# Kernel tuning notes

Hardware: AMD Instinct MI355X
Metric: run time of the kernel (lower is better)

The kernel has to match this reference:

```python
import jax, jax.numpy as jnp
import numpy as np

V, B, NT, EN, EMB, ODIM = 5000, 512, 50, 200, 200, 40
PERP = 30.0
BETA_TEMP = 0.2
SINKHORN_ALPHA = 20.0
WEIGHT_ECR = 250.0
ECR_ITERS = 100
SNE_ITERS = 20
EPS_DIV = 1e-16


def _pairwise_sq(x, y):
    # ||x_i||^2 + ||y_j||^2 - 2 x_i . y_j  (matches module's pairwise_euclidean_distance)
    return (jnp.sum(x * x, axis=1)[:, None] + jnp.sum(y * y, axis=1)[None, :]
            - 2.0 * (x @ y.T))


def _bn_train(x, g, b):
    # BatchNorm1d, training mode: batch statistics, biased variance
    m = x.mean(axis=0)
    v = x.var(axis=0)
    return (x - m) / jnp.sqrt(v + 1e-5) * g + b


def _snekhorn_reduce(X, proj):
    # SNEkhorn-style symmetric entropic affinity on rows of X (log-domain
    # symmetric Sinkhorn with uniform marginals), followed by a linear readout
    # to ODIM dims. X: (n, d) -> (n, ODIM).
    C = _pairwise_sq(X, X)                       # (n, n)
    n = X.shape[0]
    eps = jnp.mean(C) / jnp.log(PERP) + 1e-6     # bandwidth tied to perplexity
    log_a = -jnp.log(float(n))                   # uniform target marginal

    @jax.checkpoint
    def step(f, _):
        lse = jax.nn.logsumexp((f[None, :] - C) / eps, axis=1)
        f = 0.5 * (f + eps * (log_a - lse))      # symmetric Sinkhorn update
        return f, None

    f, _ = jax.lax.scan(step, jnp.zeros(n, C.dtype), None, length=SNE_ITERS)
    P = jnp.exp((f[:, None] + f[None, :] - C) / eps)  # (n, n) affinity
    return P @ proj                                   # (n, ODIM)


def _ecr_loss(cost):
    # ECR: entropic OT between topic and word embeddings (fixed-iteration Sinkhorn)
    Km = jnp.exp(-cost * SINKHORN_ALPHA)          # (NT, V)
    a = jnp.full((NT, 1), 1.0 / NT, cost.dtype)
    bm = jnp.full((V, 1), 1.0 / V, cost.dtype)

    def step(u, _):
        v = bm / (Km.T @ u + EPS_DIV)
        u = a / (Km @ v + EPS_DIV)
        return u, None

    u, _ = jax.lax.scan(step, jnp.full((NT, 1), 1.0 / NT, cost.dtype), None,
                        length=ECR_ITERS)
    v = bm / (Km.T @ u + EPS_DIV)
    transp = u * (Km * v.T)
    return WEIGHT_ECR * jnp.sum(transp * cost)


def setup_inputs() -> dict:
    key = jax.random.key(0)
    ks = jax.random.split(key, 12)

    def nrm(k, shape, s=0.02):
        return jax.random.normal(k, shape, jnp.float32) * s

    word_emb = jax.random.normal(ks[0], (V, EMB), jnp.float32)
    word_emb = word_emb / jnp.linalg.norm(word_emb, axis=1, keepdims=True)
    topic_emb = jax.random.normal(ks[1], (NT, EMB), jnp.float32) * 0.1
    topic_emb = topic_emb / jnp.linalg.norm(topic_emb, axis=1, keepdims=True)

    return dict(
        bow=jax.random.uniform(ks[2], (B, V), jnp.float32),
        eps_noise=jax.random.normal(ks[3], (ODIM, NT), jnp.float32),
        W1=nrm(ks[4], (EN, V)), b1=jnp.zeros(EN, jnp.float32),
        W2=nrm(ks[5], (EN, EN)), b2=jnp.zeros(EN, jnp.float32),
        Wmu=nrm(ks[6], (NT, EN)), bmu=jnp.zeros(NT, jnp.float32),
        Wlv=nrm(ks[7], (NT, EN)), blv=jnp.zeros(NT, jnp.float32),
        g_mu=jnp.ones(NT, jnp.float32), be_mu=jnp.zeros(NT, jnp.float32),
        g_lv=jnp.ones(NT, jnp.float32), be_lv=jnp.zeros(NT, jnp.float32),
        g_dec=jnp.ones(V, jnp.float32), be_dec=jnp.zeros(V, jnp.float32),
        word_emb=word_emb, topic_emb=topic_emb,
        proj_V=nrm(ks[8], (V, ODIM), 1.0),
        proj_K=nrm(ks[9], (NT, ODIM), 1.0),
    )


def reference(bow, eps_noise, W1, b1, W2, b2, Wmu, bmu, Wlv, blv,
              g_mu, be_mu, g_lv, be_lv, g_dec, be_dec,
              word_emb, topic_emb, proj_V, proj_K):
    # bow_reduced = SNEkhorn(bow.T).T : (ODIM, V)
    bow_reduced = _snekhorn_reduce(bow.T, proj_V).T

    # encoder1: Linear -> softplus -> Linear -> softplus
    e1 = jax.nn.softplus(bow_reduced @ W1.T + b1)
    e1 = jax.nn.softplus(e1 @ W2.T + b2)
    mu = _bn_train(e1 @ Wmu.T + bmu, g_mu, be_mu)        # (ODIM, NT)
    logvar = _bn_train(e1 @ Wlv.T + blv, g_lv, be_lv)

    z = mu + eps_noise * jnp.exp(0.5 * logvar)           # reparameterize (training)
    theta = jax.nn.softmax(z, axis=1)                    # (ODIM, NT)
    theta_reduced = _snekhorn_reduce(theta.T, proj_K).T  # (ODIM, NT)

    # KL vs logistic-normal prior; with a = ones: mu2 = 0, var2 = 1 - 1/NT
    var2 = 1.0 - 1.0 / NT
    var = jnp.exp(logvar)
    kld = 0.5 * ((var / var2 + mu * mu / var2 + jnp.log(var2) - logvar).sum(axis=1) - NT)
    loss_KL = kld.mean()

    # beta + decode (cost computed once; torch code computes it twice identically)
    cost = _pairwise_sq(topic_emb, word_emb)             # (NT, V)
    beta = jax.nn.softmax(-cost / BETA_TEMP, axis=0)
    recon = jax.nn.softmax(_bn_train(theta_reduced @ beta, g_dec, be_dec), axis=-1)
    recon_loss = -(bow_reduced * jnp.log(recon)).sum(axis=1).mean()

    loss_TM = recon_loss + loss_KL
    loss_ECR = _ecr_loss(cost)
    loss = loss_TM + loss_ECR
    return loss, loss_TM, loss_ECR, theta_reduced
```

## Files before the change

kernel.cpp:

```cpp
#include <hip/hip_runtime.h>
#include <hip/hip_bf16.h>
#include <hip/hip_fp16.h>

#define VV 5000
#define NTOP 50
#define ENH 200
#define NEMB 200
#define OD 40
#define MP 5120
#define KNS 5008

typedef __attribute__((ext_vector_type(8))) short short8;
typedef __attribute__((ext_vector_type(4))) float f32x4;

constexpr size_t OFF_R      = 0;
constexpr size_t OFF_S      = 20224;
constexpr size_t OFF_SCAL   = 22528;
constexpr size_t OFF_PHIA   = 22784;
constexpr size_t OFF_PHIB   = 43008;
constexpr size_t OFF_ROWS   = 63232;
constexpr size_t OFF_PARTS  = 63744;
constexpr size_t OFF_FLAGS  = 71936;
constexpr size_t OFF_MUPRE  = 72960;
constexpr size_t OFF_LVPRE  = 81152;
constexpr size_t OFF_E1T    = 89344;
constexpr size_t OFF_E2T    = 121600;
constexpr size_t OFF_THRED  = 153856;
constexpr size_t OFF_BOWRED = 162048;
constexpr size_t ZERO_BYTES = 962304;
constexpr size_t OFF_PVT    = 962304;
constexpr size_t OFF_XB     = 1453824;
constexpr size_t OFF_CE     = 6696704;
constexpr size_t OFF_COST   = 56696832;
constexpr size_t OFF_KM     = 57697024;
constexpr size_t OFF_BETA   = 58697216;
constexpr size_t OFF_RN     = 59697408;

__device__ __forceinline__ void ecr_block(int b, int it_base, int n_iters, bool do_final,
    const __half* __restrict__ Kn, const float* __restrict__ cost,
    float* __restrict__ acc, int* __restrict__ cnt, float* __restrict__ scal,
    char* smem){
  __half* KmL = (__half*)smem;
  float* varr = (float*)(smem + 32208);
  float* us   = (float*)(smem + 33488);
  float* p5   = (float*)(smem + 33696);
  float* redr = (float*)(smem + 34736);
  const int t = threadIdx.x;
  const int base = (b < 8) ? b*313 : 2504 + (b-8)*312;
  const int sz   = (b < 8) ? 313 : 312;
  for (int c = t; c < 322; c += 256){
    if (c < sz){
      #pragma unroll
      for (int q = 0; q < NTOP; ++q)
        KmL[q*322 + c] = Kn[(size_t)q*KNS + base + c];
    } else {
      #pragma unroll
      for (int q = 0; q < NTOP; ++q) KmL[q*322 + c] = __float2half(0.f);
    }
  }
  if (t < 52){
    float u0 = 0.f;
    if (t < NTOP){
      if (it_base == 0) u0 = 1.f/(float)NTOP;
      else {
        float sm = __hip_atomic_load(&acc[((it_base-1)%3)*64 + t],
                                     __ATOMIC_RELAXED, __HIP_MEMORY_SCOPE_AGENT);
        u0 = (1.f/(float)NTOP)/(sm + 1e-16f);
      }
    }
    us[t] = u0;
  }
  for (int c = sz + t; c < 320; c += 256) varr[c] = 0.f;
  __syncthreads();
  const bool act = (2*t < sz);
  for (int k = 0; k < n_iters; ++k){
    const int g = it_base + k;
    if (act){
      float w0 = 0.f, w1 = 0.f, w2 = 0.f, w3 = 0.f;
      #pragma unroll
      for (int q = 0; q < NTOP; q += 2){
        float u0 = us[q], u1 = us[q+1];
        float2 f0 = __half22float2(*(const __half2*)(KmL + q*322 + 2*t));
        float2 f1 = __half22float2(*(const __half2*)(KmL + (q+1)*322 + 2*t));
        w0 += f0.x*u0; w1 += f0.y*u0;
        w2 += f1.x*u1; w3 += f1.y*u1;
      }
      float2 vv;
      vv.x = (1.f/(float)VV)/((w0+w2) + 1e-16f);
      vv.y = (2*t+1 < sz) ? (1.f/(float)VV)/((w1+w3) + 1e-16f) : 0.f;
      *(float2*)(varr + 2*t) = vv;
    }
    __syncthreads();
    if (t < 250){
      const int qq = t % NTOP, stripe = t / NTOP;
      const __half* kp = KmL + qq*322 + stripe*64;
      const float* vp = varr + stripe*64;
      float s0 = 0.f, s1 = 0.f, s2 = 0.f, s3 = 0.f;
      #pragma unroll
      for (int n = 0; n < 64; n += 4){
        float2 fa = __half22float2(*(const __half2*)(kp + n));
        float2 fb = __half22float2(*(const __half2*)(kp + n + 2));
        float4 v4 = *(const float4*)(vp + n);
        s0 += fa.x*v4.x; s1 += fa.y*v4.y; s2 += fb.x*v4.z; s3 += fb.y*v4.w;
      }
      p5[stripe*52 + qq] = (s0+s1)+(s2+s3);
    }
    __syncthreads();
    if (t < NTOP){
      float sm = p5[t] + p5[52+t] + p5[104+t] + p5[156+t] + p5[208+t];
      __hip_atomic_fetch_add(&acc[(g%3)*64 + t], sm,
                             __ATOMIC_RELAXED, __HIP_MEMORY_SCOPE_AGENT);
    }
    __asm__ volatile("s_waitcnt vmcnt(0)" ::: "memory");
    if (t == 0){
      __hip_atomic_fetch_add(cnt, 1, __ATOMIC_RELEASE, __HIP_MEMORY_SCOPE_AGENT);
      const int tgt = 16*(g+1);
      while (__hip_atomic_load(cnt, __ATOMIC_ACQUIRE, __HIP_MEMORY_SCOPE_AGENT) < tgt)
        __builtin_amdgcn_s_sleep(1);
    }
    if (t < NTOP){
      float sm = __hip_atomic_load(&acc[(g%3)*64 + t],
                                   __ATOMIC_RELAXED, __HIP_MEMORY_SCOPE_AGENT);
      us[t] = (1.f/(float)NTOP)/(sm + 1e-16f);
    }
    if (t < 64)
      __hip_atomic_store(&acc[((g+2)%3)*64 + t], 0.f,
                         __ATOMIC_RELAXED, __HIP_MEMORY_SCOPE_AGENT);
    __syncthreads();
  }
  if (!do_final) return;
  float lsum = 0.f;
  if (act){
    float w0 = 0.f, w1 = 0.f, w2 = 0.f, w3 = 0.f;
    #pragma unroll
    for (int q = 0; q < NTOP; q += 2){
      float u0 = us[q], u1 = us[q+1];
      float2 f0 = __half22float2(*(const __half2*)(KmL + q*322 + 2*t));
      float2 f1 = __half22float2(*(const __half2*)(KmL + (q+1)*322 + 2*t));
      w0 += f0.x*u0; w1 += f0.y*u0;
      w2 += f1.x*u1; w3 += f1.y*u1;
    }
    float v0 = (1.f/(float)VV)/((w0+w2) + 1e-16f);
    const bool ok1 = (2*t+1 < sz);
    float v1 = ok1 ? (1.f/(float)VV)/((w1+w3) + 1e-16f) : 0.f;
    float accv = 0.f;
    #pragma unroll
    for (int q = 0; q < NTOP; ++q){
      float2 f = __half22float2(*(const __half2*)(KmL + q*322 + 2*t));
      float uq = us[q];
      float c0 = cost[(size_t)q*VV + base + 2*t];
      accv += uq*f.x*v0*c0;
      if (ok1){
        float c1 = cost[(size_t)q*VV + base + 2*t + 1];
        accv += uq*f.y*v1*c1;
      }
    }
    lsum = accv;
  }
  #pragma unroll
  for (int off = 32; off; off >>= 1) lsum += __shfl_down(lsum, off, 64);
  if ((t & 63) == 0) redr[t >> 6] = lsum;
  __syncthreads();
  if (t == 0) atomicAdd(&scal[3], redr[0]+redr[1]+redr[2]+redr[3]);
}

__global__ __launch_bounds__(256) void k1_stats(const float* __restrict__ bow,
    __hip_bfloat16* __restrict__ Xb, float* __restrict__ r, float* __restrict__ s,
    const __half* __restrict__ Kn, const float* __restrict__ cost,
    float* __restrict__ accg, int* __restrict__ cnt, float* __restrict__ scal){
  __shared__ __align__(16) char smem[34816];
  const int t = threadIdx.x;
  if (blockIdx.x >= 40){
    int b = (blockIdx.x - 40)*8 + blockIdx.y;
    ecr_block(b, 0, 15, false, Kn, cost, accg, cnt, scal, smem);
    return;
  }
  float (*lds)[129] = (float(*)[129])smem;
  const int i0 = blockIdx.x * 128, d0 = blockIdx.y * 64;
  #pragma unroll
  for (int m = 0; m < 32; ++m){
    int idx = m*256 + t;
    int di = idx >> 7;
    int ii = idx & 127;
    int gi = i0 + ii;
    lds[di][ii] = (gi < VV) ? bow[(size_t)(d0+di)*VV + gi] : 0.f;
  }
  __syncthreads();
  if (t < 128 && (i0 + t) < VV){
    float acc = 0.f;
    for (int di = 0; di < 64; ++di){ float v = lds[di][t]; acc += v*v; }
    atomicAdd(&r[i0+t], acc);
  }
  if (t < 64){
    float acc = 0.f;
    for (int ii = 0; ii < 128; ++ii) acc += lds[t][ii];
    atomicAdd(&s[d0+t], acc);
  }
  __syncthreads();
  #pragma unroll
  for (int m = 0; m < 32; ++m){
    int idx = m*256 + t;
    int ii = idx >> 6;
    int dd = idx & 63;
    Xb[(size_t)(i0+ii)*512 + d0 + dd] = __float2bfloat16(lds[dd][ii]);
  }
}

__global__ __launch_bounds__(256) void k2_eps(const float* __restrict__ r,
    const float* __restrict__ s, float* __restrict__ scal){
  const int t = threadIdx.x;
  float a = 0.f, b = 0.f;
  for (int i = t; i < VV; i += 256) a += r[i];
  for (int d = t; d < 512; d += 256){ float v = s[d]; b += v*v; }
  #pragma unroll
  for (int off = 32; off; off >>= 1){
    a += __shfl_down(a, off, 64);
    b += __shfl_down(b, off, 64);
  }
  __shared__ float ra[4], rb[4];
  int lane = t & 63, w = t >> 6;
  if (lane == 0){ ra[w] = a; rb[w] = b; }
  __syncthreads();
  if (t == 0){
    float sa = ra[0]+ra[1]+ra[2]+ra[3];
    float sb = rb[0]+rb[1]+rb[2]+rb[3];
    float meanC = 2.f*sa/(float)VV - 2.f*sb/((float)VV*(float)VV);
    float eps = meanC / logf(30.f) + 1e-6f;
    scal[0] = eps;
    scal[1] = 1.f/eps;
  }
}

__global__ __launch_bounds__(256) void k3_gemm_ecr(const __hip_bfloat16* __restrict__ Xb,
    const float* __restrict__ r, float* __restrict__ scal, __half* __restrict__ Ce,
    const __half* __restrict__ Kn, const float* __restrict__ cost,
    float* __restrict__ accg, int* __restrict__ cnt){
  __shared__ __align__(16) char smem[36864];
  if (blockIdx.x < 16){
    ecr_block(blockIdx.x, 15, 25, false, Kn, cost, accg, cnt, scal, smem);
    return;
  }
  __hip_bfloat16* As = (__hip_bfloat16*)smem;
  __hip_bfloat16* Bs = (__hip_bfloat16*)(smem + 128*72*2);
  const int b2 = blockIdx.x - 16;
  const int t = threadIdx.x;
  const int i0 = (b2 % 40) * 128, j0 = (b2 / 40) * 128;
  const int lane = t & 63, w = t >> 6;
  const int wr = w >> 1, wc = w & 1;
  const int m16 = lane & 15, q4 = lane >> 4;
  f32x4 acc[4][4];
  #pragma unroll
  for (int a = 0; a < 4; ++a)
    #pragma unroll
    for (int b = 0; b < 4; ++b) acc[a][b] = (f32x4){0.f,0.f,0.f,0.f};
  const int srow = t >> 3, sseg = t & 7;
  for (int kc = 0; kc < 512; kc += 64){
    __syncthreads();
    #pragma unroll
    for (int m = 0; m < 4; ++m){
      int row = m*32 + srow;
      uint4 va = *(const uint4*)(Xb + (size_t)(i0+row)*512 + kc + sseg*8);
      *(uint4*)(As + row*72 + sseg*8) = va;
      uint4 vb = *(const uint4*)(Xb + (size_t)(j0+row)*512 + kc + sseg*8);
      *(uint4*)(Bs + row*72 + sseg*8) = vb;
    }
    __syncthreads();
    #pragma unroll
    for (int ks = 0; ks < 64; ks += 32){
      short8 af[4], bf[4];
      #pragma unroll
      for (int f = 0; f < 4; ++f){
        af[f] = *(const short8*)(As + (wr*64 + f*16 + m16)*72 + ks + q4*8);
        bf[f] = *(const short8*)(Bs + (wc*64 + f*16 + m16)*72 + ks + q4*8);
      }
      #pragma unroll
      for (int fr = 0; fr < 4; ++fr)
        #pragma unroll
        for (int fc = 0; fc < 4; ++fc)
          acc[fr][fc] = __builtin_amdgcn_mfma_f32_16x16x32_bf16(af[fr], bf[fc], acc[fr][fc], 0, 0, 0);
    }
  }
  const float inv_eps = scal[1];
  #pragma unroll
  for (int fr = 0; fr < 4; ++fr){
    int rbase = i0 + wr*64 + fr*16 + q4*4;
    #pragma unroll
    for (int fc = 0; fc < 4; ++fc){
      int col = j0 + wc*64 + fc*16 + m16;
      if (col < VV){
        float rc = r[col];
        #pragma unroll
        for (int q = 0; q < 4; ++q){
          int row = rbase + q;
          if (row < VV){
            float val = (r[row] + rc - 2.f*acc[fr][fc][q]) * inv_eps;
            Ce[(size_t)row*VV + col] = __float2half(val);
          }
        }
      }
    }
  }
}

__global__ __launch_bounds__(256) void k4_sweep_ecr(const __half* __restrict__ Ce,
    const float* __restrict__ phi_in, float* __restrict__ phi_out,
    const __half* __restrict__ Kn, const float* __restrict__ cost,
    float* __restrict__ accg, int* __restrict__ cnt, float* __restrict__ scal,
    int it_base){
  __shared__ __align__(16) char smem[34816];
  const int t = threadIdx.x;
  if (blockIdx.x < 16){
    ecr_block(blockIdx.x, it_base, 2, false, Kn, cost, accg, cnt, scal, smem);
    return;
  }
  const int i0 = (blockIdx.x - 16) * 8;
  float acc[8];
  #pragma unroll
  for (int rr = 0; rr < 8; ++rr) acc[rr] = 0.f;
  const uint4* ce0 = (const uint4*)(Ce + (size_t)i0*VV);
  for (int u = t; u < 625; u += 256){
    float4 p0 = *(const float4*)(phi_in + u*8);
    float4 p1 = *(const float4*)(phi_in + u*8 + 4);
    #pragma unroll
    for (int rr = 0; rr < 8; ++rr){
      uint4 v = ce0[(size_t)rr*625 + u];
      const __half2* hp = (const __half2*)&v;
      float2 c0 = __half22float2(hp[0]);
      float2 c1 = __half22float2(hp[1]);
      float2 c2 = __half22float2(hp[2]);
      float2 c3 = __half22float2(hp[3]);
      acc[rr] += __expf(p0.x - c0.x) + __expf(p0.y - c0.y)
               + __expf(p0.z - c1.x) + __expf(p0.w - c1.y)
               + __expf(p1.x - c2.x) + __expf(p1.y - c2.y)
               + __expf(p1.z - c3.x) + __expf(p1.w - c3.y);
    }
  }
  #pragma unroll
  for (int rr = 0; rr < 8; ++rr)
    #pragma unroll
    for (int off = 32; off; off >>= 1)
      acc[rr] += __shfl_down(acc[rr], off, 64);
  float* red = (float*)smem;
  int lane = t & 63, w = t >> 6;
  if (lane == 0){
    #pragma unroll
    for (int rr = 0; rr < 8; ++rr) red[w*8 + rr] = acc[rr];
  }
  __syncthreads();
  if (t < 8){
    float ssum = red[t] + red[8+t] + red[16+t] + red[24+t];
    const float loga = -8.517193191416238f;
    phi_out[i0 + t] = 0.5f*(phi_in[i0 + t] + loga - __logf(ssum));
  }
}

__global__ __launch_bounds__(256) void k5p_pvt(const float* __restrict__ projV,
    __hip_bfloat16* __restrict__ pvt){
  int idx = blockIdx.x*256 + threadIdx.x;
  if (idx >= 48*MP) return;
  int n = idx / MP, j = idx - n*MP;
  float v = (n < OD && j < VV) ? projV[(size_t)j*OD + n] : 0.f;
  pvt[idx] = __float2bfloat16(v);
}

__global__ __launch_bounds__(256) void k5_bowred(const __half* __restrict__ Ce,
    const float* __restrict__ phi, const __hip_bfloat16* __restrict__ pvt,
    float* __restrict__ brpA, float* __restrict__ brpC, float* __restrict__ brpD,
    const __half* __restrict__ Kn, const float* __restrict__ cost,
    float* __restrict__ accg, int* __restrict__ cnt, float* __restrict__ scal){
  __shared__ __align__(16) char smem[34816];
  const int t = threadIdx.x;
  if (blockIdx.x >= 40){
    int b = (blockIdx.x - 40)*8 + blockIdx.y;
    ecr_block(b, 80, 15, false, Kn, cost, accg, cnt, scal, smem);
    return;
  }
  __hip_bfloat16* As = (__hip_bfloat16*)smem;
  __hip_bfloat16* Bs = (__hip_bfloat16*)(smem + 18432);
  const int i0 = blockIdx.x * 128;
  const int k0 = blockIdx.y * 640;
  const int lane = t & 63, w = t >> 6;
  const int m16 = lane & 15, q4 = lane >> 4;
  f32x4 acc[2][3];
  #pragma unroll
  for (int a = 0; a < 2; ++a)
    #pragma unroll
    for (int b = 0; b < 3; ++b) acc[a][b] = (f32x4){0.f,0.f,0.f,0.f};
  for (int kc = k0; kc < k0 + 640; kc += 64){
    __syncthreads();
    #pragma unroll
    for (int m = 0; m < 4; ++m){
      int g = m*256 + t;
      int row = g >> 3, cg = g & 7;
      int gi = i0 + row, j2 = kc + cg*8;
      union { __hip_bfloat16 h[8]; short8 v; } u;
      if (gi < VV && j2 < VV){
        uint4 vce = *(const uint4*)(Ce + (size_t)gi*VV + j2);
        const __half2* hp = (const __half2*)&vce;
        float pb = phi[gi];
        float4 pj0 = *(const float4*)(phi + j2);
        float4 pj1 = *(const float4*)(phi + j2 + 4);
        float pj[8] = {pj0.x,pj0.y,pj0.z,pj0.w,pj1.x,pj1.y,pj1.z,pj1.w};
        #pragma unroll
        for (int e = 0; e < 4; ++e){
          float2 ce = __half22float2(hp[e]);
          u.h[2*e]   = __float2bfloat16(__expf(pb + pj[2*e]   - ce.x));
          u.h[2*e+1] = __float2bfloat16(__expf(pb + pj[2*e+1] - ce.y));
        }
      } else {
        #pragma unroll
        for (int e = 0; e < 8; ++e) u.h[e] = __float2bfloat16(0.f);
      }
      *(short8*)(As + row*72 + cg*8) = u.v;
    }
    #pragma unroll
    for (int m = 0; m < 12; ++m){
      int idx = m*256 + t;
      int row = idx >> 6, c = idx & 63;
      Bs[row*72 + c] = pvt[(size_t)row*MP + kc + c];
    }
    __syncthreads();
    #pragma unroll
    for (int ks = 0; ks < 64; ks += 32){
      short8 af[2], bf[3];
      #pragma unroll
      for (int f = 0; f < 2; ++f)
        af[f] = *(const short8*)(As + (w*32 + f*16 + m16)*72 + ks + q4*8);
      #pragma unroll
      for (int f = 0; f < 3; ++f)
        bf[f] = *(const short8*)(Bs + (f*16 + m16)*72 + ks + q4*8);
      #pragma unroll
      for (int fr = 0; fr < 2; ++fr)
        #pragma unroll
        for (int fc = 0; fc < 3; ++fc)
          acc[fr][fc] = __builtin_amdgcn_mfma_f32_16x16x32_bf16(af[fr], bf[fc], acc[fr][fc], 0, 0, 0);
    }
  }
  __syncthreads();
  float* LF = (float*)smem;
  #pragma unroll
  for (int fr = 0; fr < 2; ++fr){
    int lr = w*32 + fr*16 + q4*4;
    #pragma unroll
    for (int fc = 0; fc < 3; ++fc){
      int col = fc*16 + m16;
      #pragma unroll
      for (int q = 0; q < 4; ++q)
        LF[col*133 + lr + q] = acc[fr][fc][q];
    }
  }
  __syncthreads();
  float* brp = (blockIdx.y < 6) ? brpA + (size_t)blockIdx.y*200000
             : (blockIdx.y == 6) ? brpC : brpD;
  for (int o = t; o < OD*128; o += 256){
    int col = o >> 7, row = o & 127;
    int gr = i0 + row;
    if (gr < VV) brp[(size_t)col*VV + gr] = LF[col*133 + row];
  }
}

__global__ __launch_bounds__(256) void k5r_red(const float* __restrict__ brpA,
    const float* __restrict__ brpC, const float* __restrict__ brpD,
    float* __restrict__ br){
  int idx = blockIdx.x*256 + threadIdx.x;
  if (idx >= 50000) return;
  const float4* a = (const float4*)brpA;
  float4 s = a[idx];
  #pragma unroll
  for (int sl = 1; sl < 6; ++sl){
    float4 v = a[(size_t)sl*50000 + idx];
    s.x += v.x; s.y += v.y; s.z += v.z; s.w += v.w;
  }
  {
    float4 v = ((const float4*)brpC)[idx];
    s.x += v.x; s.y += v.y; s.z += v.z; s.w += v.w;
  }
  {
    float4 v = ((const float4*)brpD)[idx];
    s.x += v.x; s.y += v.y; s.z += v.z; s.w += v.w;
  }
  ((float4*)br)[idx] = s;
}

__global__ __launch_bounds__(256) void k6_e1(const float* __restrict__ br,
    const float* __restrict__ W1, float* __restrict__ e1pre,
    const __half* __restrict__ Kn, const float* __restrict__ cost,
    float* __restrict__ accg, int* __restrict__ cnt, float* __restrict__ scal){
  __shared__ __align__(16) char smem[34816];
  const int t = threadIdx.x;
  if (blockIdx.y == 10){
    if (blockIdx.x < 16)
      ecr_block(blockIdx.x, 95, 5, true, Kn, cost, accg, cnt, scal, smem);
    return;
  }
  const int lane = t & 63, w = t >> 6;
  const int k = blockIdx.x*4 + w;
  const int f0 = blockIdx.y * 125;
  float acc[OD];
  #pragma unroll
  for (int i = 0; i < OD; ++i) acc[i] = 0.f;
  const float4* w4p = (const float4*)(W1 + (size_t)k*VV);
  for (int f4 = f0 + lane; f4 < f0 + 125; f4 += 64){
    float4 wv = w4p[f4];
    #pragma unroll
    for (int i = 0; i < OD; ++i){
      float4 bv = ((const float4*)(br + (size_t)i*VV))[f4];
      acc[i] += bv.x*wv.x + bv.y*wv.y + bv.z*wv.z + bv.w*wv.w;
    }
  }
  #pragma unroll
  for (int i = 0; i < OD; ++i)
    #pragma unroll
    for (int off = 32; off; off >>= 1)
      acc[i] += __shfl_down(acc[i], off, 64);
  float (*red)[OD] = (float(*)[OD])smem;
  if (lane == 0){
    #pragma unroll
    for (int i = 0; i < OD; ++i) red[w][i] = acc[i];
  }
  __syncthreads();
  if (t < 160){
    int ww = t / OD, i = t - ww*OD;
    int kk = blockIdx.x*4 + ww;
    atomicAdd(&e1pre[kk*OD + i], red[ww][i]);
  }
}

__global__ __launch_bounds__(256) void k6b_sp(const float* __restrict__ b1,
    float* __restrict__ e1t){
  int idx = blockIdx.x*256 + threadIdx.x;
  if (idx >= ENH*OD) return;
  int kk = idx / OD;
  float x = e1t[idx] + b1[kk];
  e1t[idx] = (x > 20.f) ? x : log1pf(__expf(x));
}

__global__ __launch_bounds__(256) void k7_e2(const float* __restrict__ e1t,
    const float* __restrict__ W2, const float* __restrict__ b2, float* __restrict__ e2t){
  const int t = threadIdx.x;
  const int lane = t & 63, w = t >> 6;
  const int k = blockIdx.x*4 + w;
  float acc[OD];
  #pragma unroll
  for (int i = 0; i < OD; ++i) acc[i] = 0.f;
  for (int j = lane; j < ENH; j += 64){
    float wv = W2[(size_t)k*ENH + j];
    #pragma unroll
    for (int i = 0; i < OD; ++i) acc[i] += e1t[j*OD + i] * wv;
  }
  #pragma unroll
  for (int i = 0; i < OD; ++i)
    #pragma unroll
    for (int off = 32; off; off >>= 1)
      acc[i] += __shfl_down(acc[i], off, 64);
  __shared__ float red[4][OD];
  if (lane == 0){
    #pragma unroll
    for (int i = 0; i < OD; ++i) red[w][i] = acc[i];
  }
  __syncthreads();
  if (t < 160){
    int ww = t / OD, i = t - ww*OD;
    int kk = blockIdx.x*4 + ww;
    float x = red[ww][i] + b2[kk];
    float sp = (x > 20.f) ? x : log1pf(__expf(x));
    e2t[kk*OD + i] = sp;
  }
}

__global__ __launch_bounds__(256) void k8a_mulv(const float* __restrict__ e2t,
    const float* __restrict__ Wmu, const float* __restrict__ bmu,
    const float* __restrict__ Wlv, const float* __restrict__ blv,
    float* __restrict__ mupre, float* __restrict__ lvpre){
  int id = blockIdx.x*256 + threadIdx.x;
  if (id >= NTOP*OD) return;
  int t50 = id / OD, i = id - t50*OD;
  float am = 0.f, al = 0.f;
  for (int kk = 0; kk < ENH; ++kk){
    float e = e2t[kk*OD + i];
    am += e * Wmu[t50*ENH + kk];
    al += e * Wlv[t50*ENH + kk];
  }
  mupre[t50*OD + i] = am + bmu[t50];
  lvpre[t50*OD + i] = al + blv[t50];
}

__global__ __launch_bounds__(256) void k8b_theta(const float* __restrict__ mupre,
    const float* __restrict__ lvpre,
    const float* __restrict__ g_mu, const float* __restrict__ be_mu,
    const float* __restrict__ g_lv, const float* __restrict__ be_lv,
    const float* __restrict__ eps_noise, const float* __restrict__ projK,
    float* __restrict__ thred, float* __restrict__ d_out3, float* __restrict__ scal){
  __shared__ float mu[NTOP][OD];
  __shared__ float lv[NTOP][OD];
  __shared__ float th[OD][NTOP];
  __shared__ float C2[NTOP][NTOP];
  __shared__ float P2[NTOP][NTOP];
  __shared__ float f2[NTOP], nf[NTOP];
  __shared__ float sred[4];
  __shared__ float eps2s[2];
  const int t = threadIdx.x;
  if (t < NTOP){
    float m = 0.f;
    for (int i = 0; i < OD; ++i) m += mupre[t*OD + i];
    m *= (1.f/OD);
    float v = 0.f;
    for (int i = 0; i < OD; ++i){ float d = mupre[t*OD+i] - m; v += d*d; }
    v *= (1.f/OD);
    float sc = g_mu[t] * rsqrtf(v + 1e-5f);
    float sh = be_mu[t];
    for (int i = 0; i < OD; ++i) mu[t][i] = (mupre[t*OD+i] - m)*sc + sh;
    m = 0.f;
    for (int i = 0; i < OD; ++i) m += lvpre[t*OD + i];
    m *= (1.f/OD);
    v = 0.f;
    for (int i = 0; i < OD; ++i){ float d = lvpre[t*OD+i] - m; v += d*d; }
    v *= (1.f/OD);
    sc = g_lv[t] * rsqrtf(v + 1e-5f);
    sh = be_lv[t];
    for (int i = 0; i < OD; ++i) lv[t][i] = (lvpre[t*OD+i] - m)*sc + sh;
  }
  __syncthreads();
  {
    float kl = 0.f;
    if (t < OD){
      const float var2 = 1.f - 1.f/(float)NTOP;
      const float lv2 = logf(var2);
      float ssum = 0.f;
      for (int q = 0; q < NTOP; ++q){
        float l = lv[q][t];
        float m = mu[q][t];
        ssum += (__expf(l) + m*m)/var2 + lv2 - l;
      }
      kl = 0.5f*(ssum - (float)NTOP);
    }
    #pragma unroll
    for (int off = 32; off; off >>= 1) kl += __shfl_down(kl, off, 64);
    if ((t & 63) == 0) sred[t >> 6] = kl;
    __syncthreads();
    if (t == 0) scal[2] = (sred[0]+sred[1]+sred[2]+sred[3]) * (1.f/OD);
    __syncthreads();
  }
  if (t < OD){
    float z[NTOP];
    float mx = -1e30f;
    for (int q = 0; q < NTOP; ++q){
      float val = mu[q][t] + eps_noise[t*NTOP + q]*__expf(0.5f*lv[q][t]);
      z[q] = val;
      mx = fmaxf(mx, val);
    }
    float ssum = 0.f;
    for (int q = 0; q < NTOP; ++q){ float e = __expf(z[q]-mx); z[q] = e; ssum += e; }
    float inv = 1.f/ssum;
    for (int q = 0; q < NTOP; ++q) th[t][q] = z[q]*inv;
  }
  __syncthreads();
  {
    float csum = 0.f;
    for (int pr = t; pr < NTOP*NTOP; pr += 256){
      int a = pr / NTOP, b = pr - (pr/NTOP)*NTOP;
      float ss = 0.f;
      for (int i = 0; i < OD; ++i){ float d = th[i][a] - th[i][b]; ss += d*d; }
      C2[a][b] = ss;
      csum += ss;
    }
    #pragma unroll
    for (int off = 32; off; off >>= 1) csum += __shfl_down(csum, off, 64);
    if ((t & 63) == 0) sred[t >> 6] = csum;
    __syncthreads();
    if (t == 0){
      float meanC = (sred[0]+sred[1]+sred[2]+sred[3]) / ((float)NTOP*NTOP);
      float e2 = meanC / logf(30.f) + 1e-6f;
      eps2s[0] = e2; eps2s[1] = 1.f/e2;
    }
  }
  if (t < NTOP) f2[t] = 0.f;
  __syncthreads();
  const float loga2 = -logf((float)NTOP);
  for (int it = 0; it < 20; ++it){
    if (t < NTOP){
      float ie = eps2s[1];
      float ssum = 0.f;
      for (int sI = 0; sI < NTOP; ++sI)
        ssum += __expf((f2[sI] - C2[t][sI]) * ie);
      float lse = __logf(ssum);
      nf[t] = 0.5f*(f2[t] + eps2s[0]*(loga2 - lse));
    }
    __syncthreads();
    if (t < NTOP) f2[t] = nf[t];
    __syncthreads();
  }
  for (int pr = t; pr < NTOP*NTOP; pr += 256){
    int a = pr / NTOP, b = pr - (pr/NTOP)*NTOP;
    P2[a][b] = __expf((f2[a] + f2[b] - C2[a][b]) * eps2s[1]);
  }
  __syncthreads();
  for (int o = t; o < NTOP*OD; o += 256){
    int t50 = o / OD, kk = o - (o/OD)*OD;
    float ssum = 0.f;
    for (int sI = 0; sI < NTOP; ++sI)
      ssum += P2[t50][sI] * projK[sI*OD + kk];
    thred[kk*NTOP + t50] = ssum;
    d_out3[kk*NTOP + t50] = ssum;
  }
}

__global__ __launch_bounds__(256) void k10_cost(const float* __restrict__ temb,
    const float* __restrict__ wemb, float* __restrict__ cost, __half* __restrict__ Kn,
    float* __restrict__ beta){
  __shared__ float Tt[100][52];
  __shared__ float wed[100][68];
  __shared__ float sc[52][64];
  __shared__ float tn[52];
  __shared__ float wn[64];
  const int t = threadIdx.x;
  const int j0 = blockIdx.x * 64;
  const int tg = t >> 4, jg = t & 15;
  float am[4][4];
  #pragma unroll
  for (int a = 0; a < 4; ++a)
    #pragma unroll
    for (int b = 0; b < 4; ++b) am[a][b] = 0.f;
  float tnp = 0.f, wnp = 0.f;
  for (int c = 0; c < 2; ++c){
    __syncthreads();
    const int dbase = c*100;
    for (int idx = t; idx < NTOP*100; idx += 256){
      int t50 = idx / 100, d = idx - t50*100;
      Tt[d][t50] = temb[t50*NEMB + dbase + d];
    }
    for (int idx = t; idx < 64*100; idx += 256){
      int j = idx / 100, d = idx - j*100;
      int gj = j0 + j;
      wed[d][j] = (gj < VV) ? wemb[(size_t)gj*NEMB + dbase + d] : 0.f;
    }
    __syncthreads();
    if (t < NTOP){
      float a = 0.f;
      for (int d = 0; d < 100; ++d){ float v = Tt[d][t]; a += v*v; }
      tnp += a;
    }
    if (t >= 64 && t < 128){
      int j = t - 64;
      float a = 0.f;
      for (int d = 0; d < 100; ++d){ float v = wed[d][j]; a += v*v; }
      wnp += a;
    }
    if (t < 208){
      for (int d = 0; d < 100; ++d){
        const float4 tv = *(const float4*)(&Tt[d][tg*4]);
        const float4 wv = *(const float4*)(&wed[d][jg*4]);
        am[0][0] += tv.x*wv.x; am[0][1] += tv.x*wv.y; am[0][2] += tv.x*wv.z; am[0][3] += tv.x*wv.w;
        am[1][0] += tv.y*wv.x; am[1][1] += tv.y*wv.y; am[1][2] += tv.y*wv.z; am[1][3] += tv.y*wv.w;
        am[2][0] += tv.z*wv.x; am[2][1] += tv.z*wv.y; am[2][2] += tv.z*wv.z; am[2][3] += tv.z*wv.w;
        am[3][0] += tv.w*wv.x; am[3][1] += tv.w*wv.y; am[3][2] += tv.w*wv.z; am[3][3] += tv.w*wv.w;
      }
    }
  }
  if (t < NTOP) tn[t] = tnp;
  if (t >= 64 && t < 128) wn[t-64] = wnp;
  __syncthreads();
  if (t < 208){
    #pragma unroll
    for (int a = 0; a < 4; ++a){
      int t50 = tg*4 + a;
      if (t50 < NTOP){
        float tv = tn[t50];
        float cc[4];
        #pragma unroll
        for (int b = 0; b < 4; ++b) cc[b] = tv + wn[jg*4+b] - 2.f*am[a][b];
        int gj = j0 + jg*4;
        if (gj + 3 < VV)
          *(float4*)(cost + (size_t)t50*VV + gj) = make_float4(cc[0],cc[1],cc[2],cc[3]);
        #pragma unroll
        for (int b = 0; b < 4; ++b) sc[t50][jg*4+b] = -5.f*cc[b];
      }
    }
  }
  __syncthreads();
  if (t < 64){
    int gj = j0 + t;
    if (gj < VV){
      float mx = -1e30f;
      for (int q = 0; q < NTOP; ++q) mx = fmaxf(mx, sc[q][t]);
      float ssum = 0.f;
      for (int q = 0; q < NTOP; ++q){ float e = __expf(sc[q][t]-mx); sc[q][t] = e; ssum += e; }
      float inv = 1.f/ssum;
      for (int q = 0; q < NTOP; ++q){
        float e = sc[q][t];
        float e2 = e*e;
        Kn[(size_t)q*KNS + gj] = __float2half(e2*e2);
        beta[(size_t)q*VV + gj] = e*inv;
      }
    }
  }
}

__global__ __launch_bounds__(256) void k12_reconA(const float* __restrict__ thred,
    const float* __restrict__ beta, const float* __restrict__ g_dec,
    const float* __restrict__ be_dec, float* __restrict__ Rn){
  __shared__ float trs[OD][NTOP];
  const int t = threadIdx.x;
  for (int o = t; o < OD*NTOP; o += 256) trs[o/NTOP][o - (o/NTOP)*NTOP] = thred[o];
  __syncthreads();
  int j = blockIdx.x*256 + t;
  if (j >= VV) return;
  float a[OD];
  #pragma unroll
  for (int i = 0; i < OD; ++i) a[i] = 0.f;
  for (int q = 0; q < NTOP; ++q){
    float bv = beta[(size_t)q*VV + j];
    #pragma unroll
    for (int i = 0; i < OD; ++i) a[i] += trs[i][q]*bv;
  }
  float m = 0.f;
  #pragma unroll
  for (int i = 0; i < OD; ++i) m += a[i];
  m *= (1.f/OD);
  float v = 0.f;
  #pragma unroll
  for (int i = 0; i < OD; ++i){ float d = a[i]-m; v += d*d; }
  v *= (1.f/OD);
  float scale = g_dec[j]*rsqrtf(v + 1e-5f);
  float sh = be_dec[j];
  #pragma unroll
  for (int i = 0; i < OD; ++i) Rn[(size_t)i*VV + j] = (a[i]-m)*scale + sh;
}

__global__ __launch_bounds__(256) void k13_reconB(const float* __restrict__ Rn,
    const float* __restrict__ br, float* __restrict__ rows){
  const int i = blockIdx.x;
  const int t = threadIdx.x;
  float s1 = 0.f, s2 = 0.f, s3 = 0.f;
  for (int j = t; j < VV; j += 256){
    float rn = Rn[(size_t)i*VV + j];
    float bv = br[(size_t)i*VV + j];
    s1 += __expf(rn);
    s2 += bv*rn;
    s3 += bv;
  }
  #pragma unroll
  for (int off = 32; off; off >>= 1){
    s1 += __shfl_down(s1, off, 64);
    s2 += __shfl_down(s2, off, 64);
    s3 += __shfl_down(s3, off, 64);
  }
  __shared__ float red[3][4];
  int lane = t & 63, w = t >> 6;
  if (lane == 0){ red[0][w] = s1; red[1][w] = s2; red[2][w] = s3; }
  __syncthreads();
  if (t == 0){
    rows[i]      = red[0][0]+red[0][1]+red[0][2]+red[0][3];
    rows[40 + i] = red[1][0]+red[1][1]+red[1][2]+red[1][3];
    rows[80 + i] = red[2][0]+red[2][1]+red[2][2]+red[2][3];
  }
}

__global__ void k14_final(const float* __restrict__ rows, const float* __restrict__ scal,
    float* __restrict__ out){
  const int t = threadIdx.x;
  float v = 0.f;
  if (t < OD) v = rows[40 + t] - logf(rows[t]) * rows[80 + t];
  #pragma unroll
  for (int off = 32; off; off >>= 1) v += __shfl_down(v, off, 64);
  if (t == 0){
    float recon = -v * (1.f/OD);
    float tm = recon + scal[2];
    float ecr = 250.f * scal[3];
    out[0] = tm + ecr;
    out[1] = tm;
    out[2] = ecr;
  }
}

extern "C" void kernel_launch(void* const* d_in, const int* in_sizes, int n_in,
                              void* d_out, int out_size, void* d_ws, size_t ws_size,
                              hipStream_t stream){
  const float* bow   = (const float*)d_in[0];
  const float* epsn  = (const float*)d_in[1];
  const float* W1    = (const float*)d_in[2];
  const float* b1    = (const float*)d_in[3];
  const float* W2    = (const float*)d_in[4];
  const float* b2    = (const float*)d_in[5];
  const float* Wmu   = (const float*)d_in[6];
  const float* bmu   = (const float*)d_in[7];
  const float* Wlv   = (const float*)d_in[8];
  const float* blv   = (const float*)d_in[9];
  const float* g_mu  = (const float*)d_in[10];
  const float* be_mu = (const float*)d_in[11];
  const float* g_lv  = (const float*)d_in[12];
  const float* be_lv = (const float*)d_in[13];
  const float* g_dec = (const float*)d_in[14];
  const float* be_dec= (const float*)d_in[15];
  const float* wemb  = (const float*)d_in[16];
  const float* temb  = (const float*)d_in[17];
  const float* projV = (const float*)d_in[18];
  const float* projK = (const float*)d_in[19];
  char* ws = (char*)d_ws;
  float* r     = (float*)(ws + OFF_R);
  float* s     = (float*)(ws + OFF_S);
  float* scal  = (float*)(ws + OFF_SCAL);
  float* phiA  = (float*)(ws + OFF_PHIA);
  float* phiB  = (float*)(ws + OFF_PHIB);
  float* rows  = (float*)(ws + OFF_ROWS);
  float* accg  = (float*)(ws + OFF_PARTS);
  int*   cnt   = (int*)(ws + OFF_FLAGS);
  float* mupre = (float*)(ws + OFF_MUPRE);
  float* lvpre = (float*)(ws + OFF_LVPRE);
  float* e1t   = (float*)(ws + OFF_E1T);
  float* e2t   = (float*)(ws + OFF_E2T);
  float* thred = (float*)(ws + OFF_THRED);
  float* br    = (float*)(ws + OFF_BOWRED);
  __hip_bfloat16* pvt = (__hip_bfloat16*)(ws + OFF_PVT);
  __hip_bfloat16* Xb  = (__hip_bfloat16*)(ws + OFF_XB);
  __half* Ce   = (__half*)(ws + OFF_CE);
  float* cost  = (float*)(ws + OFF_COST);
  __half* Kn   = (__half*)(ws + OFF_KM);
  float* beta  = (float*)(ws + OFF_BETA);
  float* Rn    = (float*)(ws + OFF_RN);
  float* brpA  = (float*)(ws + OFF_XB);
  float* brpC  = (float*)(ws + OFF_RN);
  float* brpD  = (float*)(ws + OFF_BOWRED);
  float* out   = (float*)d_out;

  hipMemsetAsync(d_ws, 0, ZERO_BYTES, stream);
  k10_cost<<<79, 256, 0, stream>>>(temb, wemb, cost, Kn, beta);
  k1_stats<<<dim3(42, 8), 256, 0, stream>>>(bow, Xb, r, s, Kn, cost, accg, cnt, scal);
  k2_eps<<<1, 256, 0, stream>>>(r, s, scal);
  k3_gemm_ecr<<<1616, 256, 0, stream>>>(Xb, r, scal, Ce, Kn, cost, accg, cnt);
  {
    float* pin = phiA; float* pout = phiB;
    for (int itr = 0; itr < 20; ++itr){
      k4_sweep_ecr<<<641, 256, 0, stream>>>(Ce, pin, pout, Kn, cost, accg, cnt,
                                            scal, 40 + 2*itr);
      float* tmp = pin; pin = pout; pout = tmp;
    }
  }
  k5p_pvt<<<960, 256, 0, stream>>>(projV, pvt);
  k5_bowred<<<dim3(42, 8), 256, 0, stream>>>(Ce, phiA, pvt, brpA, brpC, brpD,
                                             Kn, cost, accg, cnt, scal);
  k5r_red<<<196, 256, 0, stream>>>(brpA, brpC, brpD, br);
  k6_e1<<<dim3(50, 11), 256, 0, stream>>>(br, W1, e1t, Kn, cost, accg, cnt, scal);
  k6b_sp<<<32, 256, 0, stream>>>(b1, e1t);
  k7_e2<<<50, 256, 0, stream>>>(e1t, W2, b2, e2t);
  k8a_mulv<<<8, 256, 0, stream>>>(e2t, Wmu, bmu, Wlv, blv, mupre, lvpre);
  k8b_theta<<<1, 256, 0, stream>>>(mupre, lvpre, g_mu, be_mu, g_lv, be_lv,
                                   epsn, projK, thred, out + 3, scal);
  k12_reconA<<<20, 256, 0, stream>>>(thred, beta, g_dec, be_dec, Rn);
  k13_reconB<<<40, 256, 0, stream>>>(Rn, br, rows);
  k14_final<<<1, 64, 0, stream>>>(rows, scal, out);
}
```

Measured before the change: 800.4 us.

## Precompute exp(-C/eps) kernel matrix so Sinkhorn sweeps use multiply-add instead of exp

The GEMM epilogue now stores exp(-C/eps) in fp16 instead of C/eps, and each symmetric Sinkhorn sweep also writes exp(phi). The sweeps and the bow-reduction affinity then use products eb*ej*E instead of per-element exponentials. This removes roughly 25M exp evaluations per sweep; the traffic over the 5000x5000 half matrix stays the same. The ECR iteration split between k1 and k3 is also rebalanced (15/25 to 12/28). The cost is some precision: small exp(-C/eps) values can underflow in fp16.

After: 871.7 us. 8.9% more time.

```diff
diff --git a/kernel.cpp b/kernel.cpp
--- a/kernel.cpp
+++ b/kernel.cpp
@@ -35,6 +35,8 @@
 constexpr size_t OFF_KM     = 57697024;
 constexpr size_t OFF_BETA   = 58697216;
 constexpr size_t OFF_RN     = 59697408;
+constexpr size_t OFF_EYA    = OFF_RN;
+constexpr size_t OFF_EYB    = OFF_RN + 20224;
 
 __device__ __forceinline__ void ecr_block(int b, int it_base, int n_iters, bool do_final,
     const __half* __restrict__ Kn, const float* __restrict__ cost,
@@ -172,7 +174,7 @@
   const int t = threadIdx.x;
   if (blockIdx.x >= 40){
     int b = (blockIdx.x - 40)*8 + blockIdx.y;
-    ecr_block(b, 0, 15, false, Kn, cost, accg, cnt, scal, smem);
+    ecr_block(b, 0, 12, false, Kn, cost, accg, cnt, scal, smem);
     return;
   }
   float (*lds)[129] = (float(*)[129])smem;
@@ -207,8 +209,9 @@
 }
 
 __global__ __launch_bounds__(256) void k2_eps(const float* __restrict__ r,
-    const float* __restrict__ s, float* __restrict__ scal){
-  const int t = threadIdx.x;
+    const float* __restrict__ s, float* __restrict__ scal, float* __restrict__ eyA){
+  const int t = threadIdx.x;
+  for (int i = t; i < VV; i += 256) eyA[i] = 1.f;
   float a = 0.f, b = 0.f;
   for (int i = t; i < VV; i += 256) a += r[i];
   for (int d = t; d < 512; d += 256){ float v = s[d]; b += v*v; }
@@ -232,12 +235,12 @@
 }
 
 __global__ __launch_bounds__(256) void k3_gemm_ecr(const __hip_bfloat16* __restrict__ Xb,
-    const float* __restrict__ r, float* __restrict__ scal, __half* __restrict__ Ce,
+    const float* __restrict__ r, float* __restrict__ scal, __half* __restrict__ Ee,
     const __half* __restrict__ Kn, const float* __restrict__ cost,
     float* __restrict__ accg, int* __restrict__ cnt){
   __shared__ __align__(16) char smem[36864];
   if (blockIdx.x < 16){
-    ecr_block(blockIdx.x, 15, 25, false, Kn, cost, accg, cnt, scal, smem);
+    ecr_block(blockIdx.x, 12, 28, false, Kn, cost, accg, cnt, scal, smem);
     return;
   }
   __hip_bfloat16* As = (__hip_bfloat16*)smem;
@@ -294,7 +297,7 @@
           int row = rbase + q;
           if (row < VV){
             float val = (r[row] + rc - 2.f*acc[fr][fc][q]) * inv_eps;
-            Ce[(size_t)row*VV + col] = __float2half(val);
+            Ee[(size_t)row*VV + col] = __float2half(__expf(-val));
           }
         }
       }
@@ -302,8 +305,9 @@
   }
 }
 
-__global__ __launch_bounds__(256) void k4_sweep_ecr(const __half* __restrict__ Ce,
+__global__ __launch_bounds__(256) void k4_sweep_ecr(const __half* __restrict__ Ee,
     const float* __restrict__ phi_in, float* __restrict__ phi_out,
+    const float* __restrict__ ey_in, float* __restrict__ ey_out,
     const __half* __restrict__ Kn, const float* __restrict__ cost,
     float* __restrict__ accg, int* __restrict__ cnt, float* __restrict__ scal,
     int it_base){
@@ -317,10 +321,10 @@
   float acc[8];
   #pragma unroll
   for (int rr = 0; rr < 8; ++rr) acc[rr] = 0.f;
-  const uint4* ce0 = (const uint4*)(Ce + (size_t)i0*VV);
+  const uint4* ce0 = (const uint4*)(Ee + (size_t)i0*VV);
   for (int u = t; u < 625; u += 256){
-    float4 p0 = *(const float4*)(phi_in + u*8);
-    float4 p1 = *(const float4*)(phi_in + u*8 + 4);
+    float4 e0 = *(const float4*)(ey_in + u*8);
+    float4 e1 = *(const float4*)(ey_in + u*8 + 4);
     #pragma unroll
     for (int rr = 0; rr < 8; ++rr){
       uint4 v = ce0[(size_t)rr*625 + u];
@@ -329,10 +333,8 @@
       float2 c1 = __half22float2(hp[1]);
       float2 c2 = __half22float2(hp[2]);
       float2 c3 = __half22float2(hp[3]);
-      acc[rr] += __expf(p0.x - c0.x) + __expf(p0.y - c0.y)
-               + __expf(p0.z - c1.x) + __expf(p0.w - c1.y)
-               + __expf(p1.x - c2.x) + __expf(p1.y - c2.y)
-               + __expf(p1.z - c3.x) + __expf(p1.w - c3.y);
+      acc[rr] += c0.x*e0.x + c0.y*e0.y + c1.x*e0.z + c1.y*e0.w
+               + c2.x*e1.x + c2.y*e1.y + c3.x*e1.z + c3.y*e1.w;
     }
   }
   #pragma unroll
@@ -350,21 +352,32 @@
   if (t < 8){
     float ssum = red[t] + red[8+t] + red[16+t] + red[24+t];
     const float loga = -8.517193191416238f;
-    phi_out[i0 + t] = 0.5f*(phi_in[i0 + t] + loga - __logf(ssum));
+    float ph = 0.5f*(phi_in[i0 + t] + loga - __logf(ssum));
+    phi_out[i0 + t] = ph;
+    ey_out[i0 + t] = __expf(ph);
   }
 }
 
 __global__ __launch_bounds__(256) void k5p_pvt(const float* __restrict__ projV,
-    __hip_bfloat16* __restrict__ pvt){
-  int idx = blockIdx.x*256 + threadIdx.x;
+    __hip_bfloat16* __restrict__ pvt, const float* __restrict__ eyA,
+    float* __restrict__ eyf){
+  const int t = threadIdx.x;
+  if (blockIdx.x < 20){
+    if (t < 250){
+      int i = blockIdx.x*250 + t;
+      eyf[i] = eyA[i];
+    }
+    return;
+  }
+  int idx = (blockIdx.x - 20)*256 + t;
   if (idx >= 48*MP) return;
   int n = idx / MP, j = idx - n*MP;
   float v = (n < OD && j < VV) ? projV[(size_t)j*OD + n] : 0.f;
   pvt[idx] = __float2bfloat16(v);
 }
 
-__global__ __launch_bounds__(256) void k5_bowred(const __half* __restrict__ Ce,
-    const float* __restrict__ phi, const __hip_bfloat16* __restrict__ pvt,
+__global__ __launch_bounds__(256) void k5_bowred(const __half* __restrict__ Ee,
+    const float* __restrict__ eyf, const __hip_bfloat16* __restrict__ pvt,
     float* __restrict__ brpA, float* __restrict__ brpC, float* __restrict__ brpD,
     const __half* __restrict__ Kn, const float* __restrict__ cost,
     float* __restrict__ accg, int* __restrict__ cnt, float* __restrict__ scal){
@@ -395,17 +408,17 @@
       int gi = i0 + row, j2 = kc + cg*8;
       union { __hip_bfloat16 h[8]; short8 v; } u;
       if (gi < VV && j2 < VV){
-        uint4 vce = *(const uint4*)(Ce + (size_t)gi*VV + j2);
+        uint4 vce = *(const uint4*)(Ee + (size_t)gi*VV + j2);
         const __half2* hp = (const __half2*)&vce;
-        float pb = phi[gi];
-        float4 pj0 = *(const float4*)(phi + j2);
-        float4 pj1 = *(const float4*)(phi + j2 + 4);
-        float pj[8] = {pj0.x,pj0.y,pj0.z,pj0.w,pj1.x,pj1.y,pj1.z,pj1.w};
+        float eb = eyf[gi];
+        float4 ej0 = *(const float4*)(eyf + j2);
+        float4 ej1 = *(const float4*)(eyf + j2 + 4);
+        float ej[8] = {ej0.x,ej0.y,ej0.z,ej0.w,ej1.x,ej1.y,ej1.z,ej1.w};
         #pragma unroll
         for (int e = 0; e < 4; ++e){
           float2 ce = __half22float2(hp[e]);
-          u.h[2*e]   = __float2bfloat16(__expf(pb + pj[2*e]   - ce.x));
-          u.h[2*e+1] = __float2bfloat16(__expf(pb + pj[2*e+1] - ce.y));
+          u.h[2*e]   = __float2bfloat16(eb * ej[2*e]   * ce.x);
+          u.h[2*e+1] = __float2bfloat16(eb * ej[2*e+1] * ce.y);
         }
       } else {
         #pragma unroll
@@ -902,6 +915,8 @@
   float* scal  = (float*)(ws + OFF_SCAL);
   float* phiA  = (float*)(ws + OFF_PHIA);
   float* phiB  = (float*)(ws + OFF_PHIB);
+  float* eyA   = (float*)(ws + OFF_EYA);
+  float* eyB   = (float*)(ws + OFF_EYB);
   float* rows  = (float*)(ws + OFF_ROWS);
   float* accg  = (float*)(ws + OFF_PARTS);
   int*   cnt   = (int*)(ws + OFF_FLAGS);
@@ -913,7 +928,7 @@
   float* br    = (float*)(ws + OFF_BOWRED);
   __hip_bfloat16* pvt = (__hip_bfloat16*)(ws + OFF_PVT);
   __hip_bfloat16* Xb  = (__hip_bfloat16*)(ws + OFF_XB);
-  __half* Ce   = (__half*)(ws + OFF_CE);
+  __half* Ee   = (__half*)(ws + OFF_CE);
   float* cost  = (float*)(ws + OFF_COST);
   __half* Kn   = (__half*)(ws + OFF_KM);
   float* beta  = (float*)(ws + OFF_BETA);
@@ -921,23 +936,26 @@
   float* brpA  = (float*)(ws + OFF_XB);
   float* brpC  = (float*)(ws + OFF_RN);
   float* brpD  = (float*)(ws + OFF_BOWRED);
+  float* eyf   = (float*)(ws + OFF_PHIB);
   float* out   = (float*)d_out;
 
   hipMemsetAsync(d_ws, 0, ZERO_BYTES, stream);
   k10_cost<<<79, 256, 0, stream>>>(temb, wemb, cost, Kn, beta);
   k1_stats<<<dim3(42, 8), 256, 0, stream>>>(bow, Xb, r, s, Kn, cost, accg, cnt, scal);
-  k2_eps<<<1, 256, 0, stream>>>(r, s, scal);
-  k3_gemm_ecr<<<1616, 256, 0, stream>>>(Xb, r, scal, Ce, Kn, cost, accg, cnt);
+  k2_eps<<<1, 256, 0, stream>>>(r, s, scal, eyA);
+  k3_gemm_ecr<<<1616, 256, 0, stream>>>(Xb, r, scal, Ee, Kn, cost, accg, cnt);
   {
     float* pin = phiA; float* pout = phiB;
+    float* ein = eyA;  float* eout = eyB;
     for (int itr = 0; itr < 20; ++itr){
-      k4_sweep_ecr<<<641, 256, 0, stream>>>(Ce, pin, pout, Kn, cost, accg, cnt,
-                                            scal, 40 + 2*itr);
-      float* tmp = pin; pin = pout; pout = tmp;
-    }
-  }
-  k5p_pvt<<<960, 256, 0, stream>>>(projV, pvt);
-  k5_bowred<<<dim3(42, 8), 256, 0, stream>>>(Ce, phiA, pvt, brpA, brpC, brpD,
+      k4_sweep_ecr<<<641, 256, 0, stream>>>(Ee, pin, pout, ein, eout,
+                                            Kn, cost, accg, cnt, scal, 40 + 2*itr);
+      float* tp = pin; pin = pout; pout = tp;
+      float* te = ein; ein = eout; eout = te;
+    }
+  }
+  k5p_pvt<<<980, 256, 0, stream>>>(projV, pvt, eyA, eyf);
+  k5_bowred<<<dim3(42, 8), 256, 0, stream>>>(Ee, eyf, pvt, brpA, brpC, brpD,
                                              Kn, cost, accg, cnt, scal);
   k5r_red<<<196, 256, 0, stream>>>(brpA, brpC, brpD, br);
   k6_e1<<<dim3(50, 11), 256, 0, stream>>>(br, W1, e1t, Kn, cost, accg, cnt, scal);
```

## Split Sinkhorn sweep rows across two blocks with atomic partial sums

Applied to the files above, without the earlier changes.

Each 8-row block of the SNEkhorn sweep now runs as two half-column blocks that atomically add partial row sums into a triple-buffered ssum array. The phi update is deferred to the next launch, which recomputes the needed phi slice from the previous sums into shared memory, and the final update moves into k5p_pvt. This doubles the block count to fill more CUs and overlap the latency of the reductions. The cost is redundant log computation per block, atomics, and an extra memset.

After: 887.8 us. 1.11x slower.

```diff
diff --git a/kernel.cpp b/kernel.cpp
--- a/kernel.cpp
+++ b/kernel.cpp
@@ -303,24 +303,49 @@
 }
 
 __global__ __launch_bounds__(256) void k4_sweep_ecr(const __half* __restrict__ Ce,
-    const float* __restrict__ phi_in, float* __restrict__ phi_out,
+    const float* __restrict__ phi_prev, float* __restrict__ phi_cur,
+    const float* __restrict__ ssum_prev, float* __restrict__ ssum_next,
+    float* __restrict__ ssum_zero,
     const __half* __restrict__ Kn, const float* __restrict__ cost,
     float* __restrict__ accg, int* __restrict__ cnt, float* __restrict__ scal,
-    int it_base){
+    int it_base, int g){
   __shared__ __align__(16) char smem[34816];
   const int t = threadIdx.x;
   if (blockIdx.x < 16){
     ecr_block(blockIdx.x, it_base, 2, false, Kn, cost, accg, cnt, scal, smem);
     return;
   }
-  const int i0 = (blockIdx.x - 16) * 8;
+  const int sb = blockIdx.x - 16;
+  const int i0 = (sb >> 1) * 8;
+  const int h  = sb & 1;
+  const int u0 = h ? 312 : 0;
+  const int u1 = h ? 625 : 312;
+  const int jbase = u0 * 8;
+  const int ncol = (u1 - u0) * 8;
+  float* pj  = (float*)smem;
+  float* red = (float*)smem + 2504;
+  const float loga = -8.517193191416238f;
+  for (int j = t; j < ncol; j += 256){
+    int gj = jbase + j;
+    pj[j] = (g == 0) ? 0.f
+          : 0.5f*(phi_prev[gj] + loga - __logf(ssum_prev[gj]));
+  }
+  if (g > 0 && sb < 20 && t < 250){
+    int i = sb*250 + t;
+    phi_cur[i] = 0.5f*(phi_prev[i] + loga - __logf(ssum_prev[i]));
+  }
+  if (sb >= 20 && sb < 40 && t < 250)
+    ssum_zero[(sb-20)*250 + t] = 0.f;
+  __syncthreads();
   float acc[8];
   #pragma unroll
   for (int rr = 0; rr < 8; ++rr) acc[rr] = 0.f;
   const uint4* ce0 = (const uint4*)(Ce + (size_t)i0*VV);
-  for (int u = t; u < 625; u += 256){
-    float4 p0 = *(const float4*)(phi_in + u*8);
-    float4 p1 = *(const float4*)(phi_in + u*8 + 4);
+  for (int u = u0 + t; u < u1; u += 256){
+    int lj = (u - u0)*8;
+    float p[8];
+    #pragma unroll
+    for (int e = 0; e < 8; ++e) p[e] = pj[lj + e];
     #pragma unroll
     for (int rr = 0; rr < 8; ++rr){
       uint4 v = ce0[(size_t)rr*625 + u];
@@ -329,10 +354,10 @@
       float2 c1 = __half22float2(hp[1]);
       float2 c2 = __half22float2(hp[2]);
       float2 c3 = __half22float2(hp[3]);
-      acc[rr] += __expf(p0.x - c0.x) + __expf(p0.y - c0.y)
-               + __expf(p0.z - c1.x) + __expf(p0.w - c1.y)
-               + __expf(p1.x - c2.x) + __expf(p1.y - c2.y)
-               + __expf(p1.z - c3.x) + __expf(p1.w - c3.y);
+      acc[rr] += __expf(p[0] - c0.x) + __expf(p[1] - c0.y)
+               + __expf(p[2] - c1.x) + __expf(p[3] - c1.y)
+               + __expf(p[4] - c2.x) + __expf(p[5] - c2.y)
+               + __expf(p[6] - c3.x) + __expf(p[7] - c3.y);
     }
   }
   #pragma unroll
@@ -340,7 +365,6 @@
     #pragma unroll
     for (int off = 32; off; off >>= 1)
       acc[rr] += __shfl_down(acc[rr], off, 64);
-  float* red = (float*)smem;
   int lane = t & 63, w = t >> 6;
   if (lane == 0){
     #pragma unroll
@@ -348,15 +372,23 @@
   }
   __syncthreads();
   if (t < 8){
-    float ssum = red[t] + red[8+t] + red[16+t] + red[24+t];
-    const float loga = -8.517193191416238f;
-    phi_out[i0 + t] = 0.5f*(phi_in[i0 + t] + loga - __logf(ssum));
+    float psum = red[t] + red[8+t] + red[16+t] + red[24+t];
+    atomicAdd(&ssum_next[i0 + t], psum);
   }
 }
 
 __global__ __launch_bounds__(256) void k5p_pvt(const float* __restrict__ projV,
-    __hip_bfloat16* __restrict__ pvt){
-  int idx = blockIdx.x*256 + threadIdx.x;
+    __hip_bfloat16* __restrict__ pvt, const float* __restrict__ phi19,
+    const float* __restrict__ ssum19, float* __restrict__ phiF){
+  const int t = threadIdx.x;
+  if (blockIdx.x < 20){
+    if (t < 250){
+      int i = blockIdx.x*250 + t;
+      phiF[i] = 0.5f*(phi19[i] + (-8.517193191416238f) - __logf(ssum19[i]));
+    }
+    return;
+  }
+  int idx = (blockIdx.x - 20)*256 + t;
   if (idx >= 48*MP) return;
   int n = idx / MP, j = idx - n*MP;
   float v = (n < OD && j < VV) ? projV[(size_t)j*OD + n] : 0.f;
@@ -918,25 +950,29 @@
   __half* Kn   = (__half*)(ws + OFF_KM);
   float* beta  = (float*)(ws + OFF_BETA);
   float* Rn    = (float*)(ws + OFF_RN);
+  float* sbuf0 = (float*)(ws + OFF_RN);
+  float* sbuf1 = (float*)(ws + OFF_RN + 20224);
+  float* sbuf2 = (float*)(ws + OFF_RN + 40448);
+  float* sbuf[3] = {sbuf0, sbuf1, sbuf2};
+  float* P2b[2] = {phiA, phiB};
   float* brpA  = (float*)(ws + OFF_XB);
   float* brpC  = (float*)(ws + OFF_RN);
   float* brpD  = (float*)(ws + OFF_BOWRED);
   float* out   = (float*)d_out;
 
   hipMemsetAsync(d_ws, 0, ZERO_BYTES, stream);
+  hipMemsetAsync(ws + OFF_RN, 0, 60672, stream);
   k10_cost<<<79, 256, 0, stream>>>(temb, wemb, cost, Kn, beta);
   k1_stats<<<dim3(42, 8), 256, 0, stream>>>(bow, Xb, r, s, Kn, cost, accg, cnt, scal);
   k2_eps<<<1, 256, 0, stream>>>(r, s, scal);
   k3_gemm_ecr<<<1616, 256, 0, stream>>>(Xb, r, scal, Ce, Kn, cost, accg, cnt);
-  {
-    float* pin = phiA; float* pout = phiB;
-    for (int itr = 0; itr < 20; ++itr){
-      k4_sweep_ecr<<<641, 256, 0, stream>>>(Ce, pin, pout, Kn, cost, accg, cnt,
-                                            scal, 40 + 2*itr);
-      float* tmp = pin; pin = pout; pout = tmp;
-    }
-  }
-  k5p_pvt<<<960, 256, 0, stream>>>(projV, pvt);
+  for (int g = 0; g < 20; ++g){
+    k4_sweep_ecr<<<1266, 256, 0, stream>>>(Ce,
+        P2b[(g+1)&1] , P2b[g&1] ,
+        sbuf[g%3], sbuf[(g+1)%3], sbuf[(g+2)%3],
+        Kn, cost, accg, cnt, scal, 40 + 2*g, g);
+  }
+  k5p_pvt<<<980, 256, 0, stream>>>(projV, pvt, phiB, sbuf[2], phiA);
   k5_bowred<<<dim3(42, 8), 256, 0, stream>>>(Ce, phiA, pvt, brpA, brpC, brpD,
                                              Kn, cost, accg, cnt, scal);
   k5r_red<<<196, 256, 0, stream>>>(brpA, brpC, brpD, br);
```
